# Optimization experiments

Hardware: AMD Instinct MI355X
Metric: run time of the kernel (lower is better)

Reference implementation:

```python
import jax, jax.numpy as jnp
import numpy as np

H = 16
D_MODEL = 1024
D_K = D_MODEL // H
SEQ = 4096


def setup_inputs() -> dict:
    key = jax.random.key(0)
    ks = jax.random.split(key, 11)
    s = 1.0 / np.sqrt(D_MODEL)
    inp = {
        "query": jax.random.normal(ks[0], (SEQ, D_MODEL), dtype=jnp.float32),
        "key": jax.random.normal(ks[1], (SEQ, D_MODEL), dtype=jnp.float32),
        "value": jax.random.normal(ks[2], (SEQ, D_MODEL), dtype=jnp.float32),
        "Wq": jax.random.uniform(ks[3], (D_MODEL, D_MODEL), jnp.float32, -s, s),
        "bq": jax.random.uniform(ks[4], (D_MODEL,), jnp.float32, -s, s),
        "Wk": jax.random.uniform(ks[5], (D_MODEL, D_MODEL), jnp.float32, -s, s),
        "bk": jax.random.uniform(ks[6], (D_MODEL,), jnp.float32, -s, s),
        "Wv": jax.random.uniform(ks[7], (D_MODEL, D_MODEL), jnp.float32, -s, s),
        "bv": jax.random.uniform(ks[8], (D_MODEL,), jnp.float32, -s, s),
        "Wo": jax.random.uniform(ks[9], (D_MODEL, D_MODEL), jnp.float32, -s, s),
        "bo": jax.random.uniform(ks[10], (D_MODEL,), jnp.float32, -s, s),
    }
    return inp


def reference(query, key, value, Wq, bq, Wk, bk, Wv, bv, Wo, bo):
    # Linear projections (torch Linear: x @ W.T + b), then split heads.
    # [S, d_model] -> [S, h, d_k] -> [h, S, d_k]
    def proj(x, W, b):
        return (x @ W.T + b).reshape(-1, H, D_K).transpose(1, 0, 2)

    q = proj(query, Wq, bq)   # [h, S, d_k]
    k = proj(key, Wk, bk)     # [h, S, d_k]
    v = proj(value, Wv, bv)   # [h, S, d_k]

    scale = 1.0 / jnp.sqrt(jnp.asarray(D_K, dtype=q.dtype))
    scores = jnp.einsum("hnd,hmd->hnm", q, k) * scale  # [h, S, S]
    p_attn = jax.nn.softmax(scores, axis=-1)
    x = jnp.einsum("hnm,hmd->hnd", p_attn, v)           # [h, S, d_k]
    x = x.transpose(1, 0, 2).reshape(-1, H * D_K)        # [S, d_model]
    return x @ Wo.T + bo
```

## Files before the change

kernel.cpp:

```cpp
#include <hip/hip_runtime.h>
#include <hip/hip_bf16.h>
#include <stdint.h>

#define HN     16
#define DMODEL 1024
#define DKH    64
#define SEQL   4096

typedef __attribute__((ext_vector_type(8))) short bf16x8;
typedef __attribute__((ext_vector_type(4))) float f32x4;

typedef const __attribute__((address_space(1))) uint32_t gas_u32;
typedef __attribute__((address_space(3))) uint32_t las_u32;

__device__ __forceinline__ void gl_lds16(const void* g, void* l) {
  __builtin_amdgcn_global_load_lds((gas_u32*)g, (las_u32*)l, 16, 0, 0);
}

__device__ __forceinline__ unsigned short f2bf(float x) {
  uint32_t u = __float_as_uint(x);
  u = (u + 0x7fffu + ((u >> 16) & 1u)) >> 16;
  return (unsigned short)u;
}

__device__ __forceinline__ uint32_t cvt_pk_bf16(float lo, float hi) {
  uint32_t r;
  asm("v_cvt_pk_bf16_f32 %0, %1, %2" : "=v"(r) : "v"(lo), "v"(hi));
  return r;
}

__device__ __forceinline__ float fast_exp2(float x) {
  float r;
  asm("v_exp_f32 %0, %1" : "=v"(r) : "v"(x));
  return r;
}

struct CvtArgs {
  const float *q, *k, *v, *wq, *wk, *wv, *wo;
  unsigned short *qb, *kb, *vb, *wqb, *wkb, *wvb, *wob;
};

__global__ __launch_bounds__(256) void cvt_all(CvtArgs a) {
  const int stride = gridDim.x * blockDim.x;
  for (int v4 = blockIdx.x * blockDim.x + threadIdx.x; v4 < 4194304; v4 += stride) {
    const float* sp; unsigned short* dp; int idx;
    if      (v4 < 1048576) { sp = a.q;  dp = a.qb;  idx = v4; }
    else if (v4 < 2097152) { sp = a.k;  dp = a.kb;  idx = v4 - 1048576; }
    else if (v4 < 3145728) { sp = a.v;  dp = a.vb;  idx = v4 - 2097152; }
    else if (v4 < 3407872) { sp = a.wq; dp = a.wqb; idx = v4 - 3145728; }
    else if (v4 < 3670016) { sp = a.wk; dp = a.wkb; idx = v4 - 3407872; }
    else if (v4 < 3932160) { sp = a.wv; dp = a.wvb; idx = v4 - 3670016; }
    else                   { sp = a.wo; dp = a.wob; idx = v4 - 3932160; }
    float4 f = ((const float4*)sp)[idx];
    ushort4 o;
    o.x = f2bf(f.x); o.y = f2bf(f.y); o.z = f2bf(f.z); o.w = f2bf(f.w);
    ((ushort4*)dp)[idx] = o;
  }
}

struct GemmDesc {
  const unsigned short* A;
  const unsigned short* W;
  const float* bias;
  void* C;
  int mode;
};
struct GemmArgs { GemmDesc d[3]; };

__global__ __launch_bounds__(256) void gemm_bt(GemmArgs ga) {
  const GemmDesc gd = ga.d[blockIdx.z];
  constexpr int M = SEQL, N = DMODEL, K = DMODEL;
  __shared__ unsigned short As[128 * 64];
  __shared__ unsigned short Bs[128 * 64];
  const int tid = threadIdx.x;
  const int w = tid >> 6, lane = tid & 63;
  const int g16 = lane >> 4, l16 = lane & 15;
  const int wr = w >> 1, wc = w & 1;
  const int bm0 = blockIdx.y * 128, bn0 = blockIdx.x * 128;
  const int srow = tid >> 3, scc = tid & 7;

  f32x4 acc[4][4];
#pragma unroll
  for (int i = 0; i < 4; ++i)
#pragma unroll
    for (int j = 0; j < 4; ++j)
      acc[i][j] = (f32x4){0.f, 0.f, 0.f, 0.f};

  for (int k0 = 0; k0 < K; k0 += 64) {
#pragma unroll
    for (int i = 0; i < 4; ++i) {
      int row = i * 32 + srow;
      int sw = scc ^ (row & 7);
      gl_lds16(gd.A + (size_t)(bm0 + row) * K + k0 + sw * 8,
               (void*)(As + (i * 256 + w * 64) * 8));
      gl_lds16(gd.W + (size_t)(bn0 + row) * K + k0 + sw * 8,
               (void*)(Bs + (i * 256 + w * 64) * 8));
    }
    __syncthreads();
#pragma unroll
    for (int ks = 0; ks < 2; ++ks) {
      bf16x8 af[4], bfr[4];
#pragma unroll
      for (int mt = 0; mt < 4; ++mt) {
        int row = wr * 64 + mt * 16 + l16;
        af[mt] = *(const bf16x8*)&As[row * 64 + (((ks * 4 + g16) ^ (row & 7)) * 8)];
      }
#pragma unroll
      for (int nt = 0; nt < 4; ++nt) {
        int row = wc * 64 + nt * 16 + l16;
        bfr[nt] = *(const bf16x8*)&Bs[row * 64 + (((ks * 4 + g16) ^ (row & 7)) * 8)];
      }
#pragma unroll
      for (int mt = 0; mt < 4; ++mt)
#pragma unroll
        for (int nt = 0; nt < 4; ++nt)
          acc[mt][nt] = __builtin_amdgcn_mfma_f32_16x16x32_bf16(af[mt], bfr[nt], acc[mt][nt], 0, 0, 0);
    }
    __syncthreads();
  }

#pragma unroll
  for (int nt = 0; nt < 4; ++nt) {
    int col = bn0 + wc * 64 + nt * 16 + l16;
    float bcol = gd.bias[col];
#pragma unroll
    for (int mt = 0; mt < 4; ++mt) {
      int row0 = bm0 + wr * 64 + mt * 16 + g16 * 4;
      f32x4 a = acc[mt][nt];
      if (gd.mode == 0) {
        unsigned short* CB = (unsigned short*)gd.C;
#pragma unroll
        for (int r = 0; r < 4; ++r)
          CB[(size_t)(row0 + r) * N + col] = f2bf(a[r] + bcol);
      } else if (gd.mode == 1) {
        unsigned short* CT = (unsigned short*)gd.C;
        ushort4 pk;
        pk.x = f2bf(a[0] + bcol); pk.y = f2bf(a[1] + bcol);
        pk.z = f2bf(a[2] + bcol); pk.w = f2bf(a[3] + bcol);
        *(ushort4*)&CT[(size_t)col * M + row0] = pk;
      } else {
        float* CF = (float*)gd.C;
#pragma unroll
        for (int r = 0; r < 4; ++r)
          CF[(size_t)(row0 + r) * N + col] = a[r] + bcol;
      }
    }
  }
}

__global__ __launch_bounds__(256) void attn_fwd(
    const unsigned short* __restrict__ Qm, const unsigned short* __restrict__ Km,
    const unsigned short* __restrict__ Vtm, unsigned short* __restrict__ Xm) {
  __shared__ __align__(16) unsigned short Ksm[2 * 4096];
  __shared__ __align__(16) unsigned short Vsm[2 * 4096];
  __shared__ __align__(16) unsigned short Psm[4096];
  const int tid = threadIdx.x;
  const int w = tid >> 6, lane = tid & 63;
  const int g = lane >> 4, qi = lane & 15;
  const int hb = blockIdx.y * DKH;
  const int q0 = blockIdx.x * 64 + w * 16;
  const int srow = tid >> 3, scc = tid & 7;
  const float CE = 0.18033688011112042f;
  const float THR = 66.5f;

  const int r0 = srow, r1 = 32 + srow;
  const unsigned short* kp0 = Km + (size_t)r0 * DMODEL + hb + (scc ^ (r0 & 7)) * 8;
  const unsigned short* kp1 = Km + (size_t)r1 * DMODEL + hb + (scc ^ (r1 & 7)) * 8;
  const unsigned short* vp0 = Vtm + (size_t)(hb + r0) * SEQL + (scc ^ (r0 & 7)) * 8;
  const unsigned short* vp1 = Vtm + (size_t)(hb + r1) * SEQL + (scc ^ (r1 & 7)) * 8;
  unsigned short* kd0 = Ksm + (w * 64) * 8;
  unsigned short* kd1 = Ksm + (256 + w * 64) * 8;
  unsigned short* vd0 = Vsm + (w * 64) * 8;
  unsigned short* vd1 = Vsm + (256 + w * 64) * 8;

  int pw[4], pr[2];
#pragma unroll
  for (int kvt = 0; kvt < 4; ++kvt)
    pw[kvt] = w * 1024 + qi * 64 + (((2 * kvt + (g >> 1)) ^ (qi & 7)) * 8) + (g & 1) * 4;
#pragma unroll
  for (int ks = 0; ks < 2; ++ks)
    pr[ks] = w * 1024 + qi * 64 + (((ks * 4 + g) ^ (qi & 7)) * 8);

  bf16x8 qf[2];
#pragma unroll
  for (int ks = 0; ks < 2; ++ks)
    qf[ks] = *(const bf16x8*)&Qm[(size_t)(q0 + qi) * DMODEL + hb + ks * 32 + g * 8];

  f32x4 oacc[4];
#pragma unroll
  for (int i = 0; i < 4; ++i) oacc[i] = (f32x4){0.f, 0.f, 0.f, 0.f};
  float mrun = -1e30f, lsum = 0.f;

  gl_lds16(kp0, kd0); gl_lds16(kp1, kd1);
  gl_lds16(vp0, vd0); gl_lds16(vp1, vd1);
  asm volatile("s_waitcnt vmcnt(0)" ::: "memory");
  __builtin_amdgcn_s_barrier();

  int buf = 0;
  for (int t = 0; t < SEQL / 64; ++t) {
    const int tn = (t + 1) & 63;
    const int bo = (buf ^ 1) * 4096;
    gl_lds16(kp0 + (size_t)tn * 64 * DMODEL, kd0 + bo);
    gl_lds16(kp1 + (size_t)tn * 64 * DMODEL, kd1 + bo);
    gl_lds16(vp0 + tn * 64, vd0 + bo);
    gl_lds16(vp1 + tn * 64, vd1 + bo);

    const unsigned short* Kb = Ksm + buf * 4096;
    const unsigned short* Vb = Vsm + buf * 4096;

    f32x4 sv[4];
#pragma unroll
    for (int kvt = 0; kvt < 4; ++kvt) sv[kvt] = (f32x4){0.f, 0.f, 0.f, 0.f};
    __builtin_amdgcn_s_setprio(1);
#pragma unroll
    for (int kvt = 0; kvt < 4; ++kvt) {
      int row = kvt * 16 + qi;
      bf16x8 ka0 = *(const bf16x8*)&Kb[row * 64 + (((0 + g) ^ (row & 7)) * 8)];
      bf16x8 ka1 = *(const bf16x8*)&Kb[row * 64 + (((4 + g) ^ (row & 7)) * 8)];
      sv[kvt] = __builtin_amdgcn_mfma_f32_16x16x32_bf16(ka0, qf[0], sv[kvt], 0, 0, 0);
      sv[kvt] = __builtin_amdgcn_mfma_f32_16x16x32_bf16(ka1, qf[1], sv[kvt], 0, 0, 0);
    }
    __builtin_amdgcn_s_setprio(0);

    float tmax = sv[0][0];
#pragma unroll
    for (int kvt = 0; kvt < 4; ++kvt)
#pragma unroll
      for (int r = 0; r < 4; ++r) tmax = fmaxf(tmax, sv[kvt][r]);
    tmax = fmaxf(tmax, __shfl_xor(tmax, 16));
    tmax = fmaxf(tmax, __shfl_xor(tmax, 32));

    if (__any(tmax - mrun > THR)) {
      float mnew = fmaxf(mrun, tmax);
      float alpha = fast_exp2((mrun - mnew) * CE);
      lsum *= alpha;
#pragma unroll
      for (int r = 0; r < 4; ++r) {
        float ar = __shfl(alpha, (lane & 48) + g * 4 + r);
#pragma unroll
        for (int dg = 0; dg < 4; ++dg) oacc[dg][r] *= ar;
      }
      mrun = mnew;
    }

    float p[16];
    float psum = 0.f;
#pragma unroll
    for (int kvt = 0; kvt < 4; ++kvt)
#pragma unroll
      for (int r = 0; r < 4; ++r) {
        float pv = fast_exp2((sv[kvt][r] - mrun) * CE);
        p[kvt * 4 + r] = pv;
        psum += pv;
      }
    psum += __shfl_xor(psum, 16);
    psum += __shfl_xor(psum, 32);
    lsum += psum;

#pragma unroll
    for (int kvt = 0; kvt < 4; ++kvt) {
      uint2 pk;
      pk.x = cvt_pk_bf16(p[kvt * 4 + 0], p[kvt * 4 + 1]);
      pk.y = cvt_pk_bf16(p[kvt * 4 + 2], p[kvt * 4 + 3]);
      *(uint2*)&Psm[pw[kvt]] = pk;
    }
    bf16x8 pa0 = *(const bf16x8*)&Psm[pr[0]];
    bf16x8 pa1 = *(const bf16x8*)&Psm[pr[1]];

    __builtin_amdgcn_s_setprio(1);
#pragma unroll
    for (int dg = 0; dg < 4; ++dg) {
      int row = dg * 16 + qi;
      bf16x8 vb0 = *(const bf16x8*)&Vb[row * 64 + (((0 + g) ^ (row & 7)) * 8)];
      bf16x8 vb1 = *(const bf16x8*)&Vb[row * 64 + (((4 + g) ^ (row & 7)) * 8)];
      oacc[dg] = __builtin_amdgcn_mfma_f32_16x16x32_bf16(pa0, vb0, oacc[dg], 0, 0, 0);
      oacc[dg] = __builtin_amdgcn_mfma_f32_16x16x32_bf16(pa1, vb1, oacc[dg], 0, 0, 0);
    }
    __builtin_amdgcn_s_setprio(0);

    asm volatile("s_waitcnt vmcnt(0)" ::: "memory");
    __builtin_amdgcn_s_barrier();
    buf ^= 1;
  }

  float linv = 1.f / lsum;
#pragma unroll
  for (int r = 0; r < 4; ++r) {
    float lr = __shfl(linv, (lane & 48) + g * 4 + r);
    int row = q0 + g * 4 + r;
#pragma unroll
    for (int dg = 0; dg < 4; ++dg)
      Xm[(size_t)row * DMODEL + hb + dg * 16 + qi] = f2bf(oacc[dg][r] * lr);
  }
}

extern "C" void kernel_launch(void* const* d_in, const int* in_sizes, int n_in,
                              void* d_out, int out_size, void* d_ws, size_t ws_size,
                              hipStream_t stream) {
  const float* query = (const float*)d_in[0];
  const float* key_  = (const float*)d_in[1];
  const float* value = (const float*)d_in[2];
  const float* Wq = (const float*)d_in[3];
  const float* bq = (const float*)d_in[4];
  const float* Wk = (const float*)d_in[5];
  const float* bk = (const float*)d_in[6];
  const float* Wv = (const float*)d_in[7];
  const float* bv = (const float*)d_in[8];
  const float* Wo = (const float*)d_in[9];
  const float* bo = (const float*)d_in[10];

  char* ws = (char*)d_ws;
  const size_t MB = 1024 * 1024;
  unsigned short* qb  = (unsigned short*)(ws + 0 * MB);
  unsigned short* kb  = (unsigned short*)(ws + 8 * MB);
  unsigned short* vb  = (unsigned short*)(ws + 16 * MB);
  unsigned short* wqb = (unsigned short*)(ws + 24 * MB);
  unsigned short* wkb = (unsigned short*)(ws + 26 * MB);
  unsigned short* wvb = (unsigned short*)(ws + 28 * MB);
  unsigned short* wob = (unsigned short*)(ws + 30 * MB);
  unsigned short* Qp  = (unsigned short*)(ws + 32 * MB);
  unsigned short* Kp  = (unsigned short*)(ws + 40 * MB);
  unsigned short* Vtp = (unsigned short*)(ws + 48 * MB);
  unsigned short* Xp  = (unsigned short*)(ws + 56 * MB);

  CvtArgs ca{query, key_, value, Wq, Wk, Wv, Wo, qb, kb, vb, wqb, wkb, wvb, wob};
  cvt_all<<<dim3(2048), dim3(256), 0, stream>>>(ca);

  GemmArgs gp;
  gp.d[0] = GemmDesc{qb, wqb, bq, (void*)Qp, 0};
  gp.d[1] = GemmDesc{kb, wkb, bk, (void*)Kp, 0};
  gp.d[2] = GemmDesc{vb, wvb, bv, (void*)Vtp, 1};
  gemm_bt<<<dim3(8, 32, 3), dim3(256), 0, stream>>>(gp);

  attn_fwd<<<dim3(SEQL / 64, HN), dim3(256), 0, stream>>>(Qp, Kp, Vtp, Xp);

  GemmArgs go;
  go.d[0] = GemmDesc{Xp, wob, bo, d_out, 2};
  go.d[1] = go.d[0];
  go.d[2] = go.d[0];
  gemm_bt<<<dim3(8, 32, 1), dim3(256), 0, stream>>>(go);
}
```

Before: 311.4 us.

## Fold softmax scale into Q projection and compute row sums via MFMA

Moves the softmax scale and log2(e) factor into the Q projection epilogue, which removes the per-element multiply from the attention exponent. Row sums are now accumulated with an MFMA against a vector of ones, replacing the shuffle reductions. The loop is unrolled by two with precomputed LDS pointers and incrementing global pointers. The launch bound now requests 3 blocks per SM and the rescale threshold is lowered in the new exp2 units. Folding the scale in before the bf16 rounding of Q slightly changes numerics, and the row sum now comes from bf16-rounded probabilities.

```diff
diff --git a/kernel.cpp b/kernel.cpp
--- a/kernel.cpp
+++ b/kernel.cpp
@@ -64,6 +64,7 @@
   const float* bias;
   void* C;
   int mode;
+  float scale;
 };
 struct GemmArgs { GemmDesc d[3]; };
 
@@ -131,7 +132,7 @@
         unsigned short* CB = (unsigned short*)gd.C;
 #pragma unroll
         for (int r = 0; r < 4; ++r)
-          CB[(size_t)(row0 + r) * N + col] = f2bf(a[r] + bcol);
+          CB[(size_t)(row0 + r) * N + col] = f2bf((a[r] + bcol) * gd.scale);
       } else if (gd.mode == 1) {
         unsigned short* CT = (unsigned short*)gd.C;
         ushort4 pk;
@@ -148,7 +149,7 @@
   }
 }
 
-__global__ __launch_bounds__(256) void attn_fwd(
+__global__ __launch_bounds__(256, 3) void attn_fwd(
     const unsigned short* __restrict__ Qm, const unsigned short* __restrict__ Km,
     const unsigned short* __restrict__ Vtm, unsigned short* __restrict__ Xm) {
   __shared__ __align__(16) unsigned short Ksm[2 * 4096];
@@ -160,8 +161,7 @@
   const int hb = blockIdx.y * DKH;
   const int q0 = blockIdx.x * 64 + w * 16;
   const int srow = tid >> 3, scc = tid & 7;
-  const float CE = 0.18033688011112042f;
-  const float THR = 66.5f;
+  const float THR = 12.0f;
 
   const int r0 = srow, r1 = 32 + srow;
   const unsigned short* kp0 = Km + (size_t)r0 * DMODEL + hb + (scc ^ (r0 & 7)) * 8;
@@ -173,13 +173,20 @@
   unsigned short* vd0 = Vsm + (w * 64) * 8;
   unsigned short* vd1 = Vsm + (256 + w * 64) * 8;
 
-  int pw[4], pr[2];
-#pragma unroll
-  for (int kvt = 0; kvt < 4; ++kvt)
-    pw[kvt] = w * 1024 + qi * 64 + (((2 * kvt + (g >> 1)) ^ (qi & 7)) * 8) + (g & 1) * 4;
-#pragma unroll
-  for (int ks = 0; ks < 2; ++ks)
-    pr[ks] = w * 1024 + qi * 64 + (((ks * 4 + g) ^ (qi & 7)) * 8);
+  const unsigned short* kb0 = &Ksm[qi * 64 + (((0 + g) ^ (qi & 7)) * 8)];
+  const unsigned short* kb1 = &Ksm[qi * 64 + (((4 + g) ^ (qi & 7)) * 8)];
+  const unsigned short* vrb0 = &Vsm[qi * 64 + (((0 + g) ^ (qi & 7)) * 8)];
+  const unsigned short* vrb1 = &Vsm[qi * 64 + (((4 + g) ^ (qi & 7)) * 8)];
+
+  int pw0 = w * 1024 + qi * 64 + (((0 + (g >> 1)) ^ (qi & 7)) * 8) + (g & 1) * 4;
+  int pw1 = w * 1024 + qi * 64 + (((2 + (g >> 1)) ^ (qi & 7)) * 8) + (g & 1) * 4;
+  int pw2 = w * 1024 + qi * 64 + (((4 + (g >> 1)) ^ (qi & 7)) * 8) + (g & 1) * 4;
+  int pw3 = w * 1024 + qi * 64 + (((6 + (g >> 1)) ^ (qi & 7)) * 8) + (g & 1) * 4;
+  const unsigned short* prb0 = &Psm[w * 1024 + qi * 64 + (((0 + g) ^ (qi & 7)) * 8)];
+  const unsigned short* prb1 = &Psm[w * 1024 + qi * 64 + (((4 + g) ^ (qi & 7)) * 8)];
+
+  union { uint32_t u[4]; bf16x8 v; } onef;
+  onef.u[0] = onef.u[1] = onef.u[2] = onef.u[3] = 0x3F803F80u;
 
   bf16x8 qf[2];
 #pragma unroll
@@ -189,108 +196,99 @@
   f32x4 oacc[4];
 #pragma unroll
   for (int i = 0; i < 4; ++i) oacc[i] = (f32x4){0.f, 0.f, 0.f, 0.f};
-  float mrun = -1e30f, lsum = 0.f;
+  f32x4 lacc = (f32x4){0.f, 0.f, 0.f, 0.f};
+  float mrun = -1e30f;
 
   gl_lds16(kp0, kd0); gl_lds16(kp1, kd1);
   gl_lds16(vp0, vd0); gl_lds16(vp1, vd1);
+  kp0 += 64 * DMODEL; kp1 += 64 * DMODEL; vp0 += 64; vp1 += 64;
   asm volatile("s_waitcnt vmcnt(0)" ::: "memory");
   __builtin_amdgcn_s_barrier();
 
-  int buf = 0;
-  for (int t = 0; t < SEQL / 64; ++t) {
-    const int tn = (t + 1) & 63;
-    const int bo = (buf ^ 1) * 4096;
-    gl_lds16(kp0 + (size_t)tn * 64 * DMODEL, kd0 + bo);
-    gl_lds16(kp1 + (size_t)tn * 64 * DMODEL, kd1 + bo);
-    gl_lds16(vp0 + tn * 64, vd0 + bo);
-    gl_lds16(vp1 + tn * 64, vd1 + bo);
-
-    const unsigned short* Kb = Ksm + buf * 4096;
-    const unsigned short* Vb = Vsm + buf * 4096;
-
-    f32x4 sv[4];
-#pragma unroll
-    for (int kvt = 0; kvt < 4; ++kvt) sv[kvt] = (f32x4){0.f, 0.f, 0.f, 0.f};
-    __builtin_amdgcn_s_setprio(1);
-#pragma unroll
-    for (int kvt = 0; kvt < 4; ++kvt) {
-      int row = kvt * 16 + qi;
-      bf16x8 ka0 = *(const bf16x8*)&Kb[row * 64 + (((0 + g) ^ (row & 7)) * 8)];
-      bf16x8 ka1 = *(const bf16x8*)&Kb[row * 64 + (((4 + g) ^ (row & 7)) * 8)];
-      sv[kvt] = __builtin_amdgcn_mfma_f32_16x16x32_bf16(ka0, qf[0], sv[kvt], 0, 0, 0);
-      sv[kvt] = __builtin_amdgcn_mfma_f32_16x16x32_bf16(ka1, qf[1], sv[kvt], 0, 0, 0);
-    }
-    __builtin_amdgcn_s_setprio(0);
-
-    float tmax = sv[0][0];
-#pragma unroll
-    for (int kvt = 0; kvt < 4; ++kvt)
-#pragma unroll
-      for (int r = 0; r < 4; ++r) tmax = fmaxf(tmax, sv[kvt][r]);
-    tmax = fmaxf(tmax, __shfl_xor(tmax, 16));
-    tmax = fmaxf(tmax, __shfl_xor(tmax, 32));
-
-    if (__any(tmax - mrun > THR)) {
-      float mnew = fmaxf(mrun, tmax);
-      float alpha = fast_exp2((mrun - mnew) * CE);
-      lsum *= alpha;
-#pragma unroll
-      for (int r = 0; r < 4; ++r) {
-        float ar = __shfl(alpha, (lane & 48) + g * 4 + r);
-#pragma unroll
-        for (int dg = 0; dg < 4; ++dg) oacc[dg][r] *= ar;
-      }
-      mrun = mnew;
-    }
-
-    float p[16];
-    float psum = 0.f;
-#pragma unroll
-    for (int kvt = 0; kvt < 4; ++kvt)
-#pragma unroll
-      for (int r = 0; r < 4; ++r) {
-        float pv = fast_exp2((sv[kvt][r] - mrun) * CE);
-        p[kvt * 4 + r] = pv;
-        psum += pv;
-      }
-    psum += __shfl_xor(psum, 16);
-    psum += __shfl_xor(psum, 32);
-    lsum += psum;
-
-#pragma unroll
-    for (int kvt = 0; kvt < 4; ++kvt) {
-      uint2 pk;
-      pk.x = cvt_pk_bf16(p[kvt * 4 + 0], p[kvt * 4 + 1]);
-      pk.y = cvt_pk_bf16(p[kvt * 4 + 2], p[kvt * 4 + 3]);
-      *(uint2*)&Psm[pw[kvt]] = pk;
-    }
-    bf16x8 pa0 = *(const bf16x8*)&Psm[pr[0]];
-    bf16x8 pa1 = *(const bf16x8*)&Psm[pr[1]];
-
-    __builtin_amdgcn_s_setprio(1);
-#pragma unroll
-    for (int dg = 0; dg < 4; ++dg) {
-      int row = dg * 16 + qi;
-      bf16x8 vb0 = *(const bf16x8*)&Vb[row * 64 + (((0 + g) ^ (row & 7)) * 8)];
-      bf16x8 vb1 = *(const bf16x8*)&Vb[row * 64 + (((4 + g) ^ (row & 7)) * 8)];
-      oacc[dg] = __builtin_amdgcn_mfma_f32_16x16x32_bf16(pa0, vb0, oacc[dg], 0, 0, 0);
-      oacc[dg] = __builtin_amdgcn_mfma_f32_16x16x32_bf16(pa1, vb1, oacc[dg], 0, 0, 0);
-    }
-    __builtin_amdgcn_s_setprio(0);
-
-    asm volatile("s_waitcnt vmcnt(0)" ::: "memory");
-    __builtin_amdgcn_s_barrier();
-    buf ^= 1;
-  }
-
-  float linv = 1.f / lsum;
+#define ATTN_STEP(BUF)                                                         \
+  do {                                                                         \
+       \
+    gl_lds16(kp0, kd0 + ((BUF) ^ 1) * 4096);                                   \
+    gl_lds16(kp1, kd1 + ((BUF) ^ 1) * 4096);                                   \
+    gl_lds16(vp0, vd0 + ((BUF) ^ 1) * 4096);                                   \
+    gl_lds16(vp1, vd1 + ((BUF) ^ 1) * 4096);                                   \
+    kp0 += 64 * DMODEL; kp1 += 64 * DMODEL; vp0 += 64; vp1 += 64;              \
+    f32x4 sv[4];                                                               \
+    _Pragma("unroll")                                                          \
+    for (int kvt = 0; kvt < 4; ++kvt) sv[kvt] = (f32x4){0.f, 0.f, 0.f, 0.f};   \
+    __builtin_amdgcn_s_setprio(1);                                             \
+    _Pragma("unroll")                                                          \
+    for (int kvt = 0; kvt < 4; ++kvt) {                                        \
+      bf16x8 ka0 = *(const bf16x8*)(kb0 + (BUF) * 4096 + kvt * 1024);          \
+      bf16x8 ka1 = *(const bf16x8*)(kb1 + (BUF) * 4096 + kvt * 1024);          \
+      sv[kvt] = __builtin_amdgcn_mfma_f32_16x16x32_bf16(ka0, qf[0], sv[kvt], 0, 0, 0); \
+      sv[kvt] = __builtin_amdgcn_mfma_f32_16x16x32_bf16(ka1, qf[1], sv[kvt], 0, 0, 0); \
+    }                                                                          \
+    __builtin_amdgcn_s_setprio(0);                                             \
+    float tmax = sv[0][0];                                                     \
+    _Pragma("unroll")                                                          \
+    for (int kvt = 0; kvt < 4; ++kvt)                                          \
+      _Pragma("unroll")                                                        \
+      for (int r = 0; r < 4; ++r) tmax = fmaxf(tmax, sv[kvt][r]);              \
+    tmax = fmaxf(tmax, __shfl_xor(tmax, 16));                                  \
+    tmax = fmaxf(tmax, __shfl_xor(tmax, 32));                                  \
+    if (__any(tmax - mrun > THR)) {                                            \
+      float mnew = fmaxf(mrun, tmax);                                          \
+      float alpha = fast_exp2(mrun - mnew);                                    \
+      _Pragma("unroll")                                                        \
+      for (int r = 0; r < 4; ++r) {                                            \
+        float ar = __shfl(alpha, (lane & 48) + g * 4 + r);                     \
+        lacc[r] *= ar;                                                         \
+        _Pragma("unroll")                                                      \
+        for (int dg = 0; dg < 4; ++dg) oacc[dg][r] *= ar;                      \
+      }                                                                        \
+      mrun = mnew;                                                             \
+    }                                                                          \
+    float p[16];                                                               \
+    _Pragma("unroll")                                                          \
+    for (int kvt = 0; kvt < 4; ++kvt)                                          \
+      _Pragma("unroll")                                                        \
+      for (int r = 0; r < 4; ++r)                                              \
+        p[kvt * 4 + r] = fast_exp2(sv[kvt][r] - mrun);                         \
+    uint2 pk;                                                                  \
+    pk.x = cvt_pk_bf16(p[0], p[1]);  pk.y = cvt_pk_bf16(p[2], p[3]);           \
+    *(uint2*)&Psm[pw0] = pk;                                                   \
+    pk.x = cvt_pk_bf16(p[4], p[5]);  pk.y = cvt_pk_bf16(p[6], p[7]);           \
+    *(uint2*)&Psm[pw1] = pk;                                                   \
+    pk.x = cvt_pk_bf16(p[8], p[9]);  pk.y = cvt_pk_bf16(p[10], p[11]);         \
+    *(uint2*)&Psm[pw2] = pk;                                                   \
+    pk.x = cvt_pk_bf16(p[12], p[13]); pk.y = cvt_pk_bf16(p[14], p[15]);        \
+    *(uint2*)&Psm[pw3] = pk;                                                   \
+    bf16x8 pa0 = *(const bf16x8*)prb0;                                         \
+    bf16x8 pa1 = *(const bf16x8*)prb1;                                         \
+    __builtin_amdgcn_s_setprio(1);                                             \
+    lacc = __builtin_amdgcn_mfma_f32_16x16x32_bf16(pa0, onef.v, lacc, 0, 0, 0);\
+    lacc = __builtin_amdgcn_mfma_f32_16x16x32_bf16(pa1, onef.v, lacc, 0, 0, 0);\
+    _Pragma("unroll")                                                          \
+    for (int dg = 0; dg < 4; ++dg) {                                           \
+      bf16x8 vb0 = *(const bf16x8*)(vrb0 + (BUF) * 4096 + dg * 1024);          \
+      bf16x8 vb1 = *(const bf16x8*)(vrb1 + (BUF) * 4096 + dg * 1024);          \
+      oacc[dg] = __builtin_amdgcn_mfma_f32_16x16x32_bf16(pa0, vb0, oacc[dg], 0, 0, 0); \
+      oacc[dg] = __builtin_amdgcn_mfma_f32_16x16x32_bf16(pa1, vb1, oacc[dg], 0, 0, 0); \
+    }                                                                          \
+    __builtin_amdgcn_s_setprio(0);                                             \
+    asm volatile("s_waitcnt vmcnt(0)" ::: "memory");                           \
+    __builtin_amdgcn_s_barrier();                                              \
+  } while (0)
+
+  for (int tt = 0; tt < SEQL / 128; ++tt) {
+    ATTN_STEP(0);
+    ATTN_STEP(1);
+  }
+#undef ATTN_STEP
+
 #pragma unroll
   for (int r = 0; r < 4; ++r) {
-    float lr = __shfl(linv, (lane & 48) + g * 4 + r);
+    float inv = 1.f / lacc[r];
     int row = q0 + g * 4 + r;
 #pragma unroll
     for (int dg = 0; dg < 4; ++dg)
-      Xm[(size_t)row * DMODEL + hb + dg * 16 + qi] = f2bf(oacc[dg][r] * lr);
+      Xm[(size_t)row * DMODEL + hb + dg * 16 + qi] = f2bf(oacc[dg][r] * inv);
   }
 }
 
@@ -326,16 +324,17 @@
   CvtArgs ca{query, key_, value, Wq, Wk, Wv, Wo, qb, kb, vb, wqb, wkb, wvb, wob};
   cvt_all<<<dim3(2048), dim3(256), 0, stream>>>(ca);
 
+  const float CE = 0.18033688011112042f;
   GemmArgs gp;
-  gp.d[0] = GemmDesc{qb, wqb, bq, (void*)Qp, 0};
-  gp.d[1] = GemmDesc{kb, wkb, bk, (void*)Kp, 0};
-  gp.d[2] = GemmDesc{vb, wvb, bv, (void*)Vtp, 1};
+  gp.d[0] = GemmDesc{qb, wqb, bq, (void*)Qp, 0, CE};
+  gp.d[1] = GemmDesc{kb, wkb, bk, (void*)Kp, 0, 1.0f};
+  gp.d[2] = GemmDesc{vb, wvb, bv, (void*)Vtp, 1, 1.0f};
   gemm_bt<<<dim3(8, 32, 3), dim3(256), 0, stream>>>(gp);
 
   attn_fwd<<<dim3(SEQL / 64, HN), dim3(256), 0, stream>>>(Qp, Kp, Vtp, Xp);
 
   GemmArgs go;
-  go.d[0] = GemmDesc{Xp, wob, bo, d_out, 2};
+  go.d[0] = GemmDesc{Xp, wob, bo, d_out, 2, 1.0f};
   go.d[1] = go.d[0];
   go.d[2] = go.d[0];
   gemm_bt<<<dim3(8, 32, 1), dim3(256), 0, stream>>>(go);
```

Result: faster. 290.6 us (-6.7%).
